# Kernel optimization log

Hardware: AMD Instinct MI355X
Metric: run time of the kernel (lower is better)

## Reference

```python
import jax, jax.numpy as jnp
import numpy as np

# --- static config / quantization scales (simulating the torch-int modules) ---
B, S, E, H = 2, 2048, 2048, 16
D = E // H  # head_dim = 128
CATTN_ALPHA = 0.004   # W8A8B8O8Conv1D requant scale: int32 acc -> int8 out
QK_ALPHA = 1e-4       # BMM_S8T_S8N_F32T: s_q * s_k dequant scale -> fp32 logits
PV_ALPHA = 0.002      # BMM_S8T_S8N_S8T: (1/127)*s_v/s_out requant scale -> int8 out
PROJ_ALPHA = 0.003    # W8A8BFP32OFP32Conv1D dequant scale -> fp32 out


def q8(x):
    """round + saturate to int8 range (values kept in float32)."""
    return jnp.clip(jnp.round(x), -128.0, 127.0)


def setup_inputs() -> dict:
    key = jax.random.key(0)
    k0, k1, k2, k3, k4 = jax.random.split(key, 5)
    i8 = lambda k, shape: jax.random.randint(k, shape, -128, 128).astype(jnp.float32)
    return {
        "hidden_states": i8(k0, (B, S, E)),      # int8 activations (simulated)
        "w_attn": i8(k1, (E, 3 * E)),            # int8 c_attn weight (Conv1D: x @ W)
        "b_attn": i8(k2, (3 * E,)),              # int8 c_attn bias
        "w_proj": i8(k3, (E, E)),                # int8 c_proj weight
        "b_proj": jax.random.normal(k4, (E,), dtype=jnp.float32),  # fp32 c_proj bias
    }


def reference(hidden_states, w_attn, b_attn, w_proj, b_proj):
    # c_attn: W8A8B8O8 — int32 accumulate, requantize, add int8 bias, saturate
    qkv = q8(CATTN_ALPHA * jnp.matmul(hidden_states, w_attn) + b_attn)  # [B,S,3E] int8
    q, k, v = jnp.split(qkv, 3, axis=-1)

    def split_heads(t):  # [B,S,E] -> [B,H,S,D]
        return t.reshape(B, S, H, D).transpose(0, 2, 1, 3)

    q, k, v = split_heads(q), split_heads(k), split_heads(v)

    # qk_bmm: BMM_S8T_S8N_F32T -> fp32 logits, then /sqrt(head_dim)
    logits = QK_ALPHA * jnp.einsum("bhqd,bhkd->bhqk", q, k)
    logits = logits / jnp.float32(np.sqrt(D))

    # causal mask (tril bias buffer); masked positions -> dtype min
    causal = jnp.tril(jnp.ones((S, S), dtype=bool))
    mask_value = jnp.finfo(logits.dtype).min
    logits = jnp.where(causal[None, None], logits, mask_value)

    # softmax, then requantize probabilities to int8: round(p * 127)
    p = jax.nn.softmax(logits, axis=-1)
    p_i8 = q8(p * 127.0)  # [B,H,S,S] int8 (simulated)

    # pv_bmm: BMM_S8T_S8N_S8T -> int8 attn output
    attn_out = q8(PV_ALPHA * jnp.einsum("bhqk,bhkd->bhqd", p_i8, v))  # [B,H,S,D]

    # merge heads -> [B,S,E]
    attn_out = attn_out.transpose(0, 2, 1, 3).reshape(B, S, E)

    # c_proj: W8A8BFP32OFP32 — int32 accumulate, dequant to fp32, add fp32 bias
    out = PROJ_ALPHA * jnp.matmul(attn_out, w_proj) + b_proj  # [B,S,E] fp32
    return out
```

## Files before the change

### kernel.cpp

```cpp
#include <hip/hip_runtime.h>
#include <cstdint>
#include <cstddef>


typedef int v4i __attribute__((ext_vector_type(4)));

static constexpr float CATTN_ALPHA = 0.004f;
static constexpr float PV_ALPHA    = 0.002f;
static constexpr float PROJ_ALPHA  = 0.003f;
static constexpr float CE2   = 1.275174308e-05f;
static constexpr float MAGIC = 12582912.0f;

#define GLL16(gp, lp)                                              \
  __builtin_amdgcn_global_load_lds(                                \
      (const __attribute__((address_space(1))) void*)(gp),         \
      (__attribute__((address_space(3))) void*)(lp), 16, 0, 0)

__device__ __forceinline__ float exp2_fast(float x) {
#if __has_builtin(__builtin_amdgcn_exp2f)
  return __builtin_amdgcn_exp2f(x);
#else
  return __builtin_exp2f(x);
#endif
}

__device__ __forceinline__ uint32_t pack4(uint32_t u0, uint32_t u1, uint32_t u2,
                                          uint32_t u3) {
#if __has_builtin(__builtin_amdgcn_perm)
  uint32_t t01 = __builtin_amdgcn_perm(u1, u0, 0x00000400u);
  uint32_t t23 = __builtin_amdgcn_perm(u3, u2, 0x00000400u);
  return __builtin_amdgcn_perm(t23, t01, 0x05040100u);
#else
  return (u0 & 255u) | ((u1 & 255u) << 8) | ((u2 & 255u) << 16) | (u3 << 24);
#endif
}

__global__ __launch_bounds__(256) void quant_kernel(const float* __restrict__ src,
                                                    int8_t* __restrict__ dst, int n4) {
  int i = blockIdx.x * 256 + threadIdx.x;
  if (i >= n4) return;
  float4 v = reinterpret_cast<const float4*>(src)[i];
  int b0 = __float2int_rn(v.x) & 255;
  int b1 = __float2int_rn(v.y) & 255;
  int b2 = __float2int_rn(v.z) & 255;
  int b3 = __float2int_rn(v.w) & 255;
  reinterpret_cast<int*>(dst)[i] = b0 | (b1 << 8) | (b2 << 16) | (b3 << 24);
}

__global__ __launch_bounds__(256) void quant_transpose_kernel(const float* __restrict__ src,
                                                              int8_t* __restrict__ dst,
                                                              int K, int N) {
  __shared__ int8_t ts[64][68];
  const int k0 = blockIdx.x * 64, n0 = blockIdx.y * 64;
  const int t = threadIdx.x;
  for (int c = t; c < 1024; c += 256) {
    int r = c >> 4, cc = (c & 15) << 2;
    float4 v = *reinterpret_cast<const float4*>(&src[(size_t)(k0 + r) * N + n0 + cc]);
    int b0 = __float2int_rn(v.x) & 255;
    int b1 = __float2int_rn(v.y) & 255;
    int b2 = __float2int_rn(v.z) & 255;
    int b3 = __float2int_rn(v.w) & 255;
    *reinterpret_cast<int*>(&ts[r][cc]) = b0 | (b1 << 8) | (b2 << 16) | (b3 << 24);
  }
  __syncthreads();
  {
    int c = t;
    int rn = c >> 2, ck = (c & 3) << 4;
    __attribute__((aligned(16))) int8_t tmp[16];
#pragma unroll
    for (int j = 0; j < 16; ++j) tmp[j] = ts[ck + j][rn];
    *reinterpret_cast<v4i*>(&dst[(size_t)(n0 + rn) * K + k0 + ck]) =
        *reinterpret_cast<const v4i*>(tmp);
  }
}

__global__ __launch_bounds__(256) void gemm_cattn_kernel(
    const int8_t* __restrict__ A, const int8_t* __restrict__ BT,
    const float* __restrict__ bias,
    int8_t* __restrict__ qout, int8_t* __restrict__ kout, int8_t* __restrict__ vtout) {
  __shared__ __align__(16) int8_t As[2][128][128];
  __shared__ __align__(16) int8_t Bs[2][128][128];
  const int t = threadIdx.x;
  const int lane = t & 63, wave = t >> 6;
  const int wr = wave >> 1, wc = wave & 1;
  const int l15 = lane & 15, l4 = lane >> 4;
  const int m0 = blockIdx.y * 128, n0 = blockIdx.x * 128;

  const int srow = lane >> 3;
  const int scol = ((lane & 7) ^ srow) << 4;
  const int8_t* ag = A + (size_t)(m0 + wave * 32 + srow) * 2048 + scol;
  const int8_t* bg = BT + (size_t)(n0 + wave * 32 + srow) * 2048 + scol;

  auto stage = [&](int b, int ki) {
    const int8_t* a_ = ag + ki * 128;
    const int8_t* b_ = bg + ki * 128;
#pragma unroll
    for (int g = 0; g < 4; ++g) {
      GLL16(a_ + (size_t)(g * 8) * 2048, &As[b][wave * 32 + g * 8][0]);
      GLL16(b_ + (size_t)(g * 8) * 2048, &Bs[b][wave * 32 + g * 8][0]);
    }
  };

  v4i acc[4][4];
#pragma unroll
  for (int i = 0; i < 4; ++i)
#pragma unroll
    for (int j = 0; j < 4; ++j) acc[i][j] = (v4i){0, 0, 0, 0};

  const int rswz = (l4 ^ (l15 & 7)) << 4;
  const int aoff = (wr * 64 + l15) * 128 + rswz;
  const int boff = (wc * 64 + l15) * 128 + rswz;

  stage(0, 0);
  for (int ki = 0; ki < 16; ++ki) {
    if (ki < 15) {
      stage((ki + 1) & 1, ki + 1);
      asm volatile("s_waitcnt vmcnt(8)" ::: "memory");
    } else {
      asm volatile("s_waitcnt vmcnt(0)" ::: "memory");
    }
    __builtin_amdgcn_sched_barrier(0);
    __builtin_amdgcn_s_barrier();
    __builtin_amdgcn_sched_barrier(0);
    const int8_t* ab = &As[ki & 1][0][0];
    const int8_t* bb = &Bs[ki & 1][0][0];
#pragma unroll
    for (int ks = 0; ks < 2; ++ks) {
      v4i af[4], bf[4];
#pragma unroll
      for (int i = 0; i < 4; ++i)
        af[i] = *reinterpret_cast<const v4i*>(ab + ((aoff + i * 2048) ^ (ks * 64)));
#pragma unroll
      for (int j = 0; j < 4; ++j)
        bf[j] = *reinterpret_cast<const v4i*>(bb + ((boff + j * 2048) ^ (ks * 64)));
#pragma unroll
      for (int i = 0; i < 4; ++i)
#pragma unroll
        for (int j = 0; j < 4; ++j)
          acc[i][j] = __builtin_amdgcn_mfma_i32_16x16x64_i8(af[i], bf[j], acc[i][j], 0, 0, 0);
    }
    __builtin_amdgcn_sched_barrier(0);
    __builtin_amdgcn_s_barrier();
  }

  const int which = n0 >> 11;
  const int hh = (n0 & 2047) >> 7;
  const int bi = m0 >> 11;
  const int s_base = m0 & 2047;
  float bv[4];
#pragma unroll
  for (int j = 0; j < 4; ++j) bv[j] = bias[n0 + wc * 64 + j * 16 + l15];

  if (which == 2) {
    int8_t* vb = vtout + ((size_t)(bi * 16 + hh) * 128) * 2048;
#pragma unroll
    for (int i = 0; i < 4; ++i) {
#pragma unroll
      for (int j = 0; j < 4; ++j) {
        uint32_t w = 0;
#pragma unroll
        for (int rr = 0; rr < 4; ++rr) {
          float f = __fadd_rn(__fmul_rn(CATTN_ALPHA, (float)acc[i][j][rr]), bv[j]);
          f = rintf(f);
          f = fminf(fmaxf(f, -128.f), 127.f);
          w |= ((uint32_t)((int)f & 255)) << (rr * 8);
        }
        int d = wc * 64 + j * 16 + l15;
        int s0i = s_base + wr * 64 + i * 16 + l4 * 4;
        *reinterpret_cast<uint32_t*>(vb + (size_t)d * 2048 + s0i) = w;
      }
    }
  } else {
    int8_t* dst = (which == 0) ? qout : kout;
    int8_t* db = dst + ((size_t)(bi * 16 + hh) * 2048 + s_base) * 128;
#pragma unroll
    for (int i = 0; i < 4; ++i)
#pragma unroll
      for (int j = 0; j < 4; ++j)
#pragma unroll
        for (int rr = 0; rr < 4; ++rr) {
          float f = __fadd_rn(__fmul_rn(CATTN_ALPHA, (float)acc[i][j][rr]), bv[j]);
          f = rintf(f);
          f = fminf(fmaxf(f, -128.f), 127.f);
          int mo = wr * 64 + i * 16 + l4 * 4 + rr;
          int d = wc * 64 + j * 16 + l15;
          db[(size_t)mo * 128 + d] = (int8_t)(int)f;
        }
  }
}

__global__ __launch_bounds__(256) void gemm_cproj_kernel(
    const int8_t* __restrict__ A, const int8_t* __restrict__ BT,
    const float* __restrict__ bias, float* __restrict__ out) {
  __shared__ __align__(16) int8_t As[2][128][128];
  __shared__ __align__(16) int8_t Bs[2][128][128];
  const int t = threadIdx.x;
  const int lane = t & 63, wave = t >> 6;
  const int wr = wave >> 1, wc = wave & 1;
  const int l15 = lane & 15, l4 = lane >> 4;
  const int m0 = blockIdx.y * 128, n0 = blockIdx.x * 128;

  const int srow = lane >> 3;
  const int scol = ((lane & 7) ^ srow) << 4;
  const int8_t* ag = A + (size_t)(m0 + wave * 32 + srow) * 2048 + scol;
  const int8_t* bg = BT + (size_t)(n0 + wave * 32 + srow) * 2048 + scol;

  auto stage = [&](int b, int ki) {
    const int8_t* a_ = ag + ki * 128;
    const int8_t* b_ = bg + ki * 128;
#pragma unroll
    for (int g = 0; g < 4; ++g) {
      GLL16(a_ + (size_t)(g * 8) * 2048, &As[b][wave * 32 + g * 8][0]);
      GLL16(b_ + (size_t)(g * 8) * 2048, &Bs[b][wave * 32 + g * 8][0]);
    }
  };

  v4i acc[4][4];
#pragma unroll
  for (int i = 0; i < 4; ++i)
#pragma unroll
    for (int j = 0; j < 4; ++j) acc[i][j] = (v4i){0, 0, 0, 0};

  const int rswz = (l4 ^ (l15 & 7)) << 4;
  const int aoff = (wr * 64 + l15) * 128 + rswz;
  const int boff = (wc * 64 + l15) * 128 + rswz;

  stage(0, 0);
  for (int ki = 0; ki < 16; ++ki) {
    if (ki < 15) {
      stage((ki + 1) & 1, ki + 1);
      asm volatile("s_waitcnt vmcnt(8)" ::: "memory");
    } else {
      asm volatile("s_waitcnt vmcnt(0)" ::: "memory");
    }
    __builtin_amdgcn_sched_barrier(0);
    __builtin_amdgcn_s_barrier();
    __builtin_amdgcn_sched_barrier(0);
    const int8_t* ab = &As[ki & 1][0][0];
    const int8_t* bb = &Bs[ki & 1][0][0];
#pragma unroll
    for (int ks = 0; ks < 2; ++ks) {
      v4i af[4], bf[4];
#pragma unroll
      for (int i = 0; i < 4; ++i)
        af[i] = *reinterpret_cast<const v4i*>(ab + ((aoff + i * 2048) ^ (ks * 64)));
#pragma unroll
      for (int j = 0; j < 4; ++j)
        bf[j] = *reinterpret_cast<const v4i*>(bb + ((boff + j * 2048) ^ (ks * 64)));
#pragma unroll
      for (int i = 0; i < 4; ++i)
#pragma unroll
        for (int j = 0; j < 4; ++j)
          acc[i][j] = __builtin_amdgcn_mfma_i32_16x16x64_i8(af[i], bf[j], acc[i][j], 0, 0, 0);
    }
    __builtin_amdgcn_sched_barrier(0);
    __builtin_amdgcn_s_barrier();
  }
#pragma unroll
  for (int i = 0; i < 4; ++i)
#pragma unroll
    for (int j = 0; j < 4; ++j)
#pragma unroll
      for (int rr = 0; rr < 4; ++rr) {
        int m = m0 + wr * 64 + i * 16 + l4 * 4 + rr;
        int n = n0 + wc * 64 + j * 16 + l15;
        out[(size_t)m * 2048 + n] =
            __fadd_rn(__fmul_rn(PROJ_ALPHA, (float)acc[i][j][rr]), bias[n]);
      }
}

__global__ __launch_bounds__(256) void attn_kernel(
    const int8_t* __restrict__ Q, const int8_t* __restrict__ K8,
    const int8_t* __restrict__ VT, int8_t* __restrict__ O) {
  __shared__ __align__(16) int8_t q_s[64][128];
  __shared__ __align__(16) int8_t k_s[2][64][128];
  __shared__ __align__(16) int8_t vt_s[2][128][64];
  __shared__ __align__(16) int8_t p_s[64][80];

  const int t = threadIdx.x;
  const int lane = t & 63, wave = t >> 6;
  const int l15 = lane & 15, l4 = lane >> 4;
  const int bh = blockIdx.x;
  const int qt = (int)gridDim.y - 1 - (int)blockIdx.y;
  const int r0 = qt * 64;
  const size_t kqbase = (size_t)bh * (2048 * 128);
  const size_t vtbase = (size_t)bh * (128 * 2048);

  const int kq_go = ((lane >> 3) << 7) + ((((lane & 7) ^ (lane >> 3)) & 7) << 4);
  const int vt_go = ((lane >> 2) * 2048) + ((lane & 3) << 4);
  const int koff0 = (l15 << 7) + ((((0 + l4) ^ l15) & 7) << 4);
  const int koff1 = (l15 << 7) + ((((4 + l4) ^ l15) & 7) << 4);
  const int voff = l15 * 64 + l4 * 16;
  const int poff_w = (wave * 16 + l15) * 80 + l4 * 4;
  const int poff_r = (wave * 16 + l15) * 80 + l4 * 16;

  {
    const int8_t* qg = Q + kqbase + (size_t)(r0 + wave * 16) * 128 + kq_go;
    GLL16(qg, &q_s[wave * 16][0]);
    GLL16(qg + 8 * 128, &q_s[wave * 16 + 8][0]);
    const int8_t* kg = K8 + kqbase + (size_t)(wave * 16) * 128 + kq_go;
    GLL16(kg, &k_s[0][wave * 16][0]);
    GLL16(kg + 8 * 128, &k_s[0][wave * 16 + 8][0]);
  }
  __syncthreads();

  const v4i qf0 = *reinterpret_cast<const v4i*>(&q_s[0][0] + wave * 2048 + koff0);
  const v4i qf1 = *reinterpret_cast<const v4i*>(&q_s[0][0] + wave * 2048 + koff1);
  const int qgl = wave * 16 + l15;

  float acc_l[4] = {0.f, 0.f, 0.f, 0.f};

  for (int tt = 0; tt <= qt; ++tt) {
    if (tt < qt) {
      const int8_t* kg =
          K8 + kqbase + (size_t)((tt + 1) * 64 + wave * 16) * 128 + kq_go;
      GLL16(kg, &k_s[(tt + 1) & 1][wave * 16][0]);
      GLL16(kg + 8 * 128, &k_s[(tt + 1) & 1][wave * 16 + 8][0]);
    }
    const int8_t* kb = &k_s[tt & 1][0][0];
    v4i sacc[4];
#pragma unroll
    for (int ni = 0; ni < 4; ++ni) sacc[ni] = (v4i){0, 0, 0, 0};
#pragma unroll
    for (int ni = 0; ni < 4; ++ni) {
      v4i ak = *reinterpret_cast<const v4i*>(kb + ni * 2048 + koff0);
      sacc[ni] = __builtin_amdgcn_mfma_i32_16x16x64_i8(ak, qf0, sacc[ni], 0, 0, 0);
    }
#pragma unroll
    for (int ni = 0; ni < 4; ++ni) {
      v4i ak = *reinterpret_cast<const v4i*>(kb + ni * 2048 + koff1);
      sacc[ni] = __builtin_amdgcn_mfma_i32_16x16x64_i8(ak, qf1, sacc[ni], 0, 0, 0);
    }
    if (tt < qt) {
#pragma unroll
      for (int ni = 0; ni < 4; ++ni)
#pragma unroll
        for (int rr = 0; rr < 4; ++rr)
          acc_l[rr] += exp2_fast(CE2 * (float)sacc[ni][rr]);
    } else {
#pragma unroll
      for (int ni = 0; ni < 4; ++ni)
#pragma unroll
        for (int rr = 0; rr < 4; ++rr) {
          float e = exp2_fast(CE2 * (float)sacc[ni][rr]);
          acc_l[rr] += (ni * 16 + l4 * 4 + rr <= qgl) ? e : 0.f;
        }
    }
    __syncthreads();
  }
  float l_run = (acc_l[0] + acc_l[1]) + (acc_l[2] + acc_l[3]);
  l_run += __shfl_xor(l_run, 16);
  l_run += __shfl_xor(l_run, 32);
  const float inv = 127.0f / l_run;

  {
    const int8_t* kg = K8 + kqbase + (size_t)(wave * 16) * 128 + kq_go;
    GLL16(kg, &k_s[0][wave * 16][0]);
    GLL16(kg + 8 * 128, &k_s[0][wave * 16 + 8][0]);
    const int8_t* vg = VT + vtbase + (size_t)(wave * 32) * 2048 + vt_go;
    GLL16(vg, &vt_s[0][wave * 32][0]);
    GLL16(vg + (size_t)16 * 2048, &vt_s[0][wave * 32 + 16][0]);
  }
  __syncthreads();

  v4i oacc[8];
#pragma unroll
  for (int nj = 0; nj < 8; ++nj) oacc[nj] = (v4i){0, 0, 0, 0};

  for (int tt = 0; tt <= qt; ++tt) {
    if (tt < qt) {
      const int kb1 = (tt + 1) * 64;
      const int8_t* kg = K8 + kqbase + (size_t)(kb1 + wave * 16) * 128 + kq_go;
      GLL16(kg, &k_s[(tt + 1) & 1][wave * 16][0]);
      GLL16(kg + 8 * 128, &k_s[(tt + 1) & 1][wave * 16 + 8][0]);
      const int8_t* vg = VT + vtbase + (size_t)(wave * 32) * 2048 + kb1 + vt_go;
      GLL16(vg, &vt_s[(tt + 1) & 1][wave * 32][0]);
      GLL16(vg + (size_t)16 * 2048, &vt_s[(tt + 1) & 1][wave * 32 + 16][0]);
    }
    const int8_t* kb = &k_s[tt & 1][0][0];
    v4i sacc[4];
#pragma unroll
    for (int ni = 0; ni < 4; ++ni) sacc[ni] = (v4i){0, 0, 0, 0};
#pragma unroll
    for (int ni = 0; ni < 4; ++ni) {
      v4i ak = *reinterpret_cast<const v4i*>(kb + ni * 2048 + koff0);
      sacc[ni] = __builtin_amdgcn_mfma_i32_16x16x64_i8(ak, qf0, sacc[ni], 0, 0, 0);
    }
#pragma unroll
    for (int ni = 0; ni < 4; ++ni) {
      v4i ak = *reinterpret_cast<const v4i*>(kb + ni * 2048 + koff1);
      sacc[ni] = __builtin_amdgcn_mfma_i32_16x16x64_i8(ak, qf1, sacc[ni], 0, 0, 0);
    }
    if (tt < qt) {
#pragma unroll
      for (int ni = 0; ni < 4; ++ni) {
        float f0 = fmaf(exp2_fast(CE2 * (float)sacc[ni][0]), inv, MAGIC);
        float f1 = fmaf(exp2_fast(CE2 * (float)sacc[ni][1]), inv, MAGIC);
        float f2 = fmaf(exp2_fast(CE2 * (float)sacc[ni][2]), inv, MAGIC);
        float f3 = fmaf(exp2_fast(CE2 * (float)sacc[ni][3]), inv, MAGIC);
        uint32_t w = pack4(__float_as_uint(f0), __float_as_uint(f1),
                           __float_as_uint(f2), __float_as_uint(f3));
        *reinterpret_cast<uint32_t*>(&p_s[0][0] + poff_w + ni * 16) = w;
      }
    } else {
#pragma unroll
      for (int ni = 0; ni < 4; ++ni) {
        float e0 = exp2_fast(CE2 * (float)sacc[ni][0]);
        float e1 = exp2_fast(CE2 * (float)sacc[ni][1]);
        float e2 = exp2_fast(CE2 * (float)sacc[ni][2]);
        float e3 = exp2_fast(CE2 * (float)sacc[ni][3]);
        int c = ni * 16 + l4 * 4;
        e0 = (c + 0 <= qgl) ? e0 : 0.f;
        e1 = (c + 1 <= qgl) ? e1 : 0.f;
        e2 = (c + 2 <= qgl) ? e2 : 0.f;
        e3 = (c + 3 <= qgl) ? e3 : 0.f;
        float f0 = fmaf(e0, inv, MAGIC), f1 = fmaf(e1, inv, MAGIC);
        float f2 = fmaf(e2, inv, MAGIC), f3 = fmaf(e3, inv, MAGIC);
        uint32_t w = pack4(__float_as_uint(f0), __float_as_uint(f1),
                           __float_as_uint(f2), __float_as_uint(f3));
        *reinterpret_cast<uint32_t*>(&p_s[0][0] + poff_w + ni * 16) = w;
      }
    }
    asm volatile("s_waitcnt lgkmcnt(0)" ::: "memory");
    v4i pf = *reinterpret_cast<const v4i*>(&p_s[0][0] + poff_r);
    const int8_t* vb = &vt_s[tt & 1][0][0];
#pragma unroll
    for (int nj = 0; nj < 8; ++nj) {
      v4i vf = *reinterpret_cast<const v4i*>(vb + nj * 1024 + voff);
      oacc[nj] = __builtin_amdgcn_mfma_i32_16x16x64_i8(pf, vf, oacc[nj], 0, 0, 0);
    }
    __syncthreads();
  }

  const int bq = bh >> 4, hh = bh & 15;
#pragma unroll
  for (int nj = 0; nj < 8; ++nj) {
#pragma unroll
    for (int rr = 0; rr < 4; ++rr) {
      int r = r0 + wave * 16 + l4 * 4 + rr;
      int d = nj * 16 + l15;
      float f = rintf(__fmul_rn(PV_ALPHA, (float)oacc[nj][rr]));
      f = fminf(fmaxf(f, -128.f), 127.f);
      O[((size_t)bq * 2048 + r) * 2048 + hh * 128 + d] = (int8_t)(int)f;
    }
  }
}

extern "C" void kernel_launch(void* const* d_in, const int* in_sizes, int n_in,
                              void* d_out, int out_size, void* d_ws, size_t ws_size,
                              hipStream_t stream) {
  const float* hs_f    = (const float*)d_in[0];
  const float* wattn_f = (const float*)d_in[1];
  const float* battn_f = (const float*)d_in[2];
  const float* wproj_f = (const float*)d_in[3];
  const float* bproj_f = (const float*)d_in[4];
  float* out_f = (float*)d_out;

  int8_t* ws = (int8_t*)d_ws;
  int8_t* hs_i8   = ws;
  int8_t* wT_attn = ws + 8388608;
  int8_t* wT_proj = ws + 20971520;
  int8_t* q_i8    = ws + 25165824;
  int8_t* k_i8    = ws + 33554432;
  int8_t* vT_i8   = ws + 41943040;
  int8_t* attn_i8 = ws + 50331648;

  quant_kernel<<<dim3(8192), dim3(256), 0, stream>>>(hs_f, hs_i8, 2097152);
  quant_transpose_kernel<<<dim3(32, 96), dim3(256), 0, stream>>>(wattn_f, wT_attn, 2048, 6144);
  quant_transpose_kernel<<<dim3(32, 32), dim3(256), 0, stream>>>(wproj_f, wT_proj, 2048, 2048);
  gemm_cattn_kernel<<<dim3(48, 32), dim3(256), 0, stream>>>(hs_i8, wT_attn, battn_f,
                                                            q_i8, k_i8, vT_i8);
  attn_kernel<<<dim3(32, 32), dim3(256), 0, stream>>>(q_i8, k_i8, vT_i8, attn_i8);
  gemm_cproj_kernel<<<dim3(16, 32), dim3(256), 0, stream>>>(attn_i8, wT_proj, bproj_f, out_f);
}
```

Baseline: 168.3 us.

## Use 128-row query tiles with 8 waves in attention to share K/V loads

Result: slower. 173.1 us (+2.9%).

```diff
diff --git a/kernel.cpp b/kernel.cpp
--- a/kernel.cpp
+++ b/kernel.cpp
@@ -33,6 +33,13 @@
 #else
   return (u0 & 255u) | ((u1 & 255u) << 8) | ((u2 & 255u) << 16) | (u3 << 24);
 #endif
+}
+
+__device__ __forceinline__ uint32_t rq8(float alpha, int a, float b) {
+  float f = __fadd_rn(__fmul_rn(alpha, (float)a), b);
+  f = rintf(f);
+  f = fminf(fmaxf(f, -128.f), 127.f);
+  return (uint32_t)((int)f) & 255u;
 }
 
 __global__ __launch_bounds__(256) void quant_kernel(const float* __restrict__ src,
@@ -157,14 +164,10 @@
     for (int i = 0; i < 4; ++i) {
 #pragma unroll
       for (int j = 0; j < 4; ++j) {
-        uint32_t w = 0;
-#pragma unroll
-        for (int rr = 0; rr < 4; ++rr) {
-          float f = __fadd_rn(__fmul_rn(CATTN_ALPHA, (float)acc[i][j][rr]), bv[j]);
-          f = rintf(f);
-          f = fminf(fmaxf(f, -128.f), 127.f);
-          w |= ((uint32_t)((int)f & 255)) << (rr * 8);
-        }
+        uint32_t w = pack4(rq8(CATTN_ALPHA, acc[i][j][0], bv[j]),
+                           rq8(CATTN_ALPHA, acc[i][j][1], bv[j]),
+                           rq8(CATTN_ALPHA, acc[i][j][2], bv[j]),
+                           rq8(CATTN_ALPHA, acc[i][j][3], bv[j]));
         int d = wc * 64 + j * 16 + l15;
         int s0i = s_base + wr * 64 + i * 16 + l4 * 4;
         *reinterpret_cast<uint32_t*>(vb + (size_t)d * 2048 + s0i) = w;
@@ -269,20 +272,21 @@
       }
 }
 
-__global__ __launch_bounds__(256) void attn_kernel(
+__global__ __launch_bounds__(512) void attn_kernel(
     const int8_t* __restrict__ Q, const int8_t* __restrict__ K8,
     const int8_t* __restrict__ VT, int8_t* __restrict__ O) {
-  __shared__ __align__(16) int8_t q_s[64][128];
+  __shared__ __align__(16) int8_t q_s[128][128];
   __shared__ __align__(16) int8_t k_s[2][64][128];
   __shared__ __align__(16) int8_t vt_s[2][128][64];
-  __shared__ __align__(16) int8_t p_s[64][80];
+  __shared__ __align__(16) int8_t p_s[128][80];
 
   const int t = threadIdx.x;
   const int lane = t & 63, wave = t >> 6;
   const int l15 = lane & 15, l4 = lane >> 4;
   const int bh = blockIdx.x;
   const int qt = (int)gridDim.y - 1 - (int)blockIdx.y;
-  const int r0 = qt * 64;
+  const int r0 = qt * 128;
+  const int ntiles = 2 * qt + 2;
   const size_t kqbase = (size_t)bh * (2048 * 128);
   const size_t vtbase = (size_t)bh * (128 * 2048);
 
@@ -298,24 +302,23 @@
     const int8_t* qg = Q + kqbase + (size_t)(r0 + wave * 16) * 128 + kq_go;
     GLL16(qg, &q_s[wave * 16][0]);
     GLL16(qg + 8 * 128, &q_s[wave * 16 + 8][0]);
-    const int8_t* kg = K8 + kqbase + (size_t)(wave * 16) * 128 + kq_go;
-    GLL16(kg, &k_s[0][wave * 16][0]);
-    GLL16(kg + 8 * 128, &k_s[0][wave * 16 + 8][0]);
+    const int8_t* kg = K8 + kqbase + (size_t)(wave * 8) * 128 + kq_go;
+    GLL16(kg, &k_s[0][wave * 8][0]);
   }
   __syncthreads();
 
   const v4i qf0 = *reinterpret_cast<const v4i*>(&q_s[0][0] + wave * 2048 + koff0);
   const v4i qf1 = *reinterpret_cast<const v4i*>(&q_s[0][0] + wave * 2048 + koff1);
-  const int qgl = wave * 16 + l15;
+  const int wqmin = r0 + wave * 16;
 
   float acc_l[4] = {0.f, 0.f, 0.f, 0.f};
 
-  for (int tt = 0; tt <= qt; ++tt) {
-    if (tt < qt) {
+  for (int tt = 0; tt < ntiles; ++tt) {
+    const int kbase = tt * 64;
+    if (tt < ntiles - 1) {
       const int8_t* kg =
-          K8 + kqbase + (size_t)((tt + 1) * 64 + wave * 16) * 128 + kq_go;
-      GLL16(kg, &k_s[(tt + 1) & 1][wave * 16][0]);
-      GLL16(kg + 8 * 128, &k_s[(tt + 1) & 1][wave * 16 + 8][0]);
+          K8 + kqbase + (size_t)((tt + 1) * 64 + wave * 8) * 128 + kq_go;
+      GLL16(kg, &k_s[(tt + 1) & 1][wave * 8][0]);
     }
     const int8_t* kb = &k_s[tt & 1][0][0];
     v4i sacc[4];
@@ -331,19 +334,20 @@
       v4i ak = *reinterpret_cast<const v4i*>(kb + ni * 2048 + koff1);
       sacc[ni] = __builtin_amdgcn_mfma_i32_16x16x64_i8(ak, qf1, sacc[ni], 0, 0, 0);
     }
-    if (tt < qt) {
+    if (kbase + 63 <= wqmin) {
 #pragma unroll
       for (int ni = 0; ni < 4; ++ni)
 #pragma unroll
         for (int rr = 0; rr < 4; ++rr)
           acc_l[rr] += exp2_fast(CE2 * (float)sacc[ni][rr]);
     } else {
+      const int qrel = wqmin + l15 - kbase;
 #pragma unroll
       for (int ni = 0; ni < 4; ++ni)
 #pragma unroll
         for (int rr = 0; rr < 4; ++rr) {
           float e = exp2_fast(CE2 * (float)sacc[ni][rr]);
-          acc_l[rr] += (ni * 16 + l4 * 4 + rr <= qgl) ? e : 0.f;
+          acc_l[rr] += (ni * 16 + l4 * 4 + rr <= qrel) ? e : 0.f;
         }
     }
     __syncthreads();
@@ -354,12 +358,10 @@
   const float inv = 127.0f / l_run;
 
   {
-    const int8_t* kg = K8 + kqbase + (size_t)(wave * 16) * 128 + kq_go;
-    GLL16(kg, &k_s[0][wave * 16][0]);
-    GLL16(kg + 8 * 128, &k_s[0][wave * 16 + 8][0]);
-    const int8_t* vg = VT + vtbase + (size_t)(wave * 32) * 2048 + vt_go;
-    GLL16(vg, &vt_s[0][wave * 32][0]);
-    GLL16(vg + (size_t)16 * 2048, &vt_s[0][wave * 32 + 16][0]);
+    const int8_t* kg = K8 + kqbase + (size_t)(wave * 8) * 128 + kq_go;
+    GLL16(kg, &k_s[0][wave * 8][0]);
+    const int8_t* vg = VT + vtbase + (size_t)(wave * 16) * 2048 + vt_go;
+    GLL16(vg, &vt_s[0][wave * 16][0]);
   }
   __syncthreads();
 
@@ -367,15 +369,14 @@
 #pragma unroll
   for (int nj = 0; nj < 8; ++nj) oacc[nj] = (v4i){0, 0, 0, 0};
 
-  for (int tt = 0; tt <= qt; ++tt) {
-    if (tt < qt) {
+  for (int tt = 0; tt < ntiles; ++tt) {
+    const int kbase = tt * 64;
+    if (tt < ntiles - 1) {
       const int kb1 = (tt + 1) * 64;
-      const int8_t* kg = K8 + kqbase + (size_t)(kb1 + wave * 16) * 128 + kq_go;
-      GLL16(kg, &k_s[(tt + 1) & 1][wave * 16][0]);
-      GLL16(kg + 8 * 128, &k_s[(tt + 1) & 1][wave * 16 + 8][0]);
-      const int8_t* vg = VT + vtbase + (size_t)(wave * 32) * 2048 + kb1 + vt_go;
-      GLL16(vg, &vt_s[(tt + 1) & 1][wave * 32][0]);
-      GLL16(vg + (size_t)16 * 2048, &vt_s[(tt + 1) & 1][wave * 32 + 16][0]);
+      const int8_t* kg = K8 + kqbase + (size_t)(kb1 + wave * 8) * 128 + kq_go;
+      GLL16(kg, &k_s[(tt + 1) & 1][wave * 8][0]);
+      const int8_t* vg = VT + vtbase + (size_t)(wave * 16) * 2048 + kb1 + vt_go;
+      GLL16(vg, &vt_s[(tt + 1) & 1][wave * 16][0]);
     }
     const int8_t* kb = &k_s[tt & 1][0][0];
     v4i sacc[4];
@@ -391,7 +392,7 @@
       v4i ak = *reinterpret_cast<const v4i*>(kb + ni * 2048 + koff1);
       sacc[ni] = __builtin_amdgcn_mfma_i32_16x16x64_i8(ak, qf1, sacc[ni], 0, 0, 0);
     }
-    if (tt < qt) {
+    if (kbase + 63 <= wqmin) {
 #pragma unroll
       for (int ni = 0; ni < 4; ++ni) {
         float f0 = fmaf(exp2_fast(CE2 * (float)sacc[ni][0]), inv, MAGIC);
@@ -403,6 +404,7 @@
         *reinterpret_cast<uint32_t*>(&p_s[0][0] + poff_w + ni * 16) = w;
       }
     } else {
+      const int qrel = wqmin + l15 - kbase;
 #pragma unroll
       for (int ni = 0; ni < 4; ++ni) {
         float e0 = exp2_fast(CE2 * (float)sacc[ni][0]);
@@ -410,10 +412,10 @@
         float e2 = exp2_fast(CE2 * (float)sacc[ni][2]);
         float e3 = exp2_fast(CE2 * (float)sacc[ni][3]);
         int c = ni * 16 + l4 * 4;
-        e0 = (c + 0 <= qgl) ? e0 : 0.f;
-        e1 = (c + 1 <= qgl) ? e1 : 0.f;
-        e2 = (c + 2 <= qgl) ? e2 : 0.f;
-        e3 = (c + 3 <= qgl) ? e3 : 0.f;
+        e0 = (c + 0 <= qrel) ? e0 : 0.f;
+        e1 = (c + 1 <= qrel) ? e1 : 0.f;
+        e2 = (c + 2 <= qrel) ? e2 : 0.f;
+        e3 = (c + 3 <= qrel) ? e3 : 0.f;
         float f0 = fmaf(e0, inv, MAGIC), f1 = fmaf(e1, inv, MAGIC);
         float f2 = fmaf(e2, inv, MAGIC), f3 = fmaf(e3, inv, MAGIC);
         uint32_t w = pack4(__float_as_uint(f0), __float_as_uint(f1),
@@ -427,21 +429,22 @@
 #pragma unroll
     for (int nj = 0; nj < 8; ++nj) {
       v4i vf = *reinterpret_cast<const v4i*>(vb + nj * 1024 + voff);
-      oacc[nj] = __builtin_amdgcn_mfma_i32_16x16x64_i8(pf, vf, oacc[nj], 0, 0, 0);
+      oacc[nj] = __builtin_amdgcn_mfma_i32_16x16x64_i8(vf, pf, oacc[nj], 0, 0, 0);
     }
     __syncthreads();
   }
 
   const int bq = bh >> 4, hh = bh & 15;
-#pragma unroll
-  for (int nj = 0; nj < 8; ++nj) {
-#pragma unroll
-    for (int rr = 0; rr < 4; ++rr) {
-      int r = r0 + wave * 16 + l4 * 4 + rr;
-      int d = nj * 16 + l15;
-      float f = rintf(__fmul_rn(PV_ALPHA, (float)oacc[nj][rr]));
-      f = fminf(fmaxf(f, -128.f), 127.f);
-      O[((size_t)bq * 2048 + r) * 2048 + hh * 128 + d] = (int8_t)(int)f;
+  {
+    int r = r0 + wave * 16 + l15;
+    int8_t* ob = O + ((size_t)bq * 2048 + r) * 2048 + hh * 128;
+#pragma unroll
+    for (int nj = 0; nj < 8; ++nj) {
+      uint32_t w = pack4(rq8(PV_ALPHA, oacc[nj][0], 0.f),
+                         rq8(PV_ALPHA, oacc[nj][1], 0.f),
+                         rq8(PV_ALPHA, oacc[nj][2], 0.f),
+                         rq8(PV_ALPHA, oacc[nj][3], 0.f));
+      *reinterpret_cast<uint32_t*>(ob + nj * 16 + l4 * 4) = w;
     }
   }
 }
@@ -470,6 +473,6 @@
   quant_transpose_kernel<<<dim3(32, 32), dim3(256), 0, stream>>>(wproj_f, wT_proj, 2048, 2048);
   gemm_cattn_kernel<<<dim3(48, 32), dim3(256), 0, stream>>>(hs_i8, wT_attn, battn_f,
                                                             q_i8, k_i8, vT_i8);
-  attn_kernel<<<dim3(32, 32), dim3(256), 0, stream>>>(q_i8, k_i8, vT_i8, attn_i8);
+  attn_kernel<<<dim3(32, 16), dim3(512), 0, stream>>>(q_i8, k_i8, vT_i8, attn_i8);
   gemm_cproj_kernel<<<dim3(16, 32), dim3(256), 0, stream>>>(attn_i8, wT_proj, bproj_f, out_f);
 }
```
